# Kernel tuning notes

Measured on AMD Instinct MI355X. Metric: run time of the kernel, lower is better.

The kernel has to match this reference:

```python
import jax, jax.numpy as jnp
import numpy as np


def setup_inputs() -> dict:
    key = jax.random.key(0)
    k1, k2 = jax.random.split(key)
    B, P, C, N = 32, 3, 512, 1024
    input_data1 = jax.random.normal(k1, (B, P, C, N), dtype=jnp.float32)
    input_data2 = jax.random.normal(k2, (B, P, C, N), dtype=jnp.float32)
    return {"input_data1": input_data1, "input_data2": input_data2}


def reference(input_data1, input_data2):
    # HorizontalComparisonModel.compare_algorithm_method4 (the only path used):
    # permute [B,P,C,N] -> [B,P,N,C], reshape to [B, P*N, C] pairs of C-dim vectors.
    B = input_data1.shape[0]
    x = jnp.transpose(input_data1, (0, 1, 3, 2)).reshape(B, -1, input_data1.shape[2])
    y = jnp.transpose(input_data2, (0, 1, 3, 2)).reshape(B, -1, input_data2.shape[2])
    d = x - y                                   # [B, pairs, C]
    l1 = jnp.sum(jnp.abs(d), axis=-1)           # temp31: L1 distance
    sq_l2 = jnp.sum(d * d, axis=-1)             # temp21: squared L2 distance
    # Original stacks [temp31, temp21, temp31] (L1 appears twice; cosine unused).
    out = jnp.stack([l1, sq_l2, l1], axis=-1)   # [B, pairs, 3]
    return out.reshape(B, -1)
```

## Files before the change

kernel.cpp:

```cpp
#include <hip/hip_runtime.h>

constexpr int B = 32, P = 3, C = 512, N = 1024;
constexpr int G = B * P;
constexpr int CSPLIT = 16;
constexpr int CCHUNK = C / CSPLIT;
constexpr size_t WS_NEED = (size_t)CSPLIT * G * N * 2 * sizeof(float);

__global__ __launch_bounds__(256) void dist_partial(
    const float* __restrict__ x1, const float* __restrict__ x2,
    float* __restrict__ ws)
{
    const int g     = blockIdx.x / CSPLIT;
    const int chunk = blockIdx.x % CSPLIT;
    const int t     = threadIdx.x;

    const float4* pa = (const float4*)(x1 + (size_t)g * C * N)
                       + (size_t)chunk * CCHUNK * (N / 4) + t;
    const float4* pb = (const float4*)(x2 + (size_t)g * C * N)
                       + (size_t)chunk * CCHUNK * (N / 4) + t;

    float4 l1 = make_float4(0.f, 0.f, 0.f, 0.f);
    float4 l2 = make_float4(0.f, 0.f, 0.f, 0.f);

    #pragma unroll
    for (int j = 0; j < CCHUNK; j += 4) {
        const float4 a0 = pa[0 * (N / 4)];
        const float4 a1 = pa[1 * (N / 4)];
        const float4 a2 = pa[2 * (N / 4)];
        const float4 a3 = pa[3 * (N / 4)];
        const float4 b0 = pb[0 * (N / 4)];
        const float4 b1 = pb[1 * (N / 4)];
        const float4 b2 = pb[2 * (N / 4)];
        const float4 b3 = pb[3 * (N / 4)];
        pa += N;
        pb += N;
        float d;
        d = a0.x - b0.x; l1.x += fabsf(d); l2.x = fmaf(d, d, l2.x);
        d = a0.y - b0.y; l1.y += fabsf(d); l2.y = fmaf(d, d, l2.y);
        d = a0.z - b0.z; l1.z += fabsf(d); l2.z = fmaf(d, d, l2.z);
        d = a0.w - b0.w; l1.w += fabsf(d); l2.w = fmaf(d, d, l2.w);
        d = a1.x - b1.x; l1.x += fabsf(d); l2.x = fmaf(d, d, l2.x);
        d = a1.y - b1.y; l1.y += fabsf(d); l2.y = fmaf(d, d, l2.y);
        d = a1.z - b1.z; l1.z += fabsf(d); l2.z = fmaf(d, d, l2.z);
        d = a1.w - b1.w; l1.w += fabsf(d); l2.w = fmaf(d, d, l2.w);
        d = a2.x - b2.x; l1.x += fabsf(d); l2.x = fmaf(d, d, l2.x);
        d = a2.y - b2.y; l1.y += fabsf(d); l2.y = fmaf(d, d, l2.y);
        d = a2.z - b2.z; l1.z += fabsf(d); l2.z = fmaf(d, d, l2.z);
        d = a2.w - b2.w; l1.w += fabsf(d); l2.w = fmaf(d, d, l2.w);
        d = a3.x - b3.x; l1.x += fabsf(d); l2.x = fmaf(d, d, l2.x);
        d = a3.y - b3.y; l1.y += fabsf(d); l2.y = fmaf(d, d, l2.y);
        d = a3.z - b3.z; l1.z += fabsf(d); l2.z = fmaf(d, d, l2.z);
        d = a3.w - b3.w; l1.w += fabsf(d); l2.w = fmaf(d, d, l2.w);
    }

    float4* wout = (float4*)ws + ((size_t)(chunk * G + g) * N) / 2 + 2 * t;
    wout[0] = make_float4(l1.x, l2.x, l1.y, l2.y);
    wout[1] = make_float4(l1.z, l2.z, l1.w, l2.w);
}

__global__ __launch_bounds__(256) void dist_combine(
    const float* __restrict__ ws, float* __restrict__ out)
{
    const int idx = blockIdx.x * 256 + threadIdx.x;
    const float2* ws2 = (const float2*)ws;
    float l1 = 0.f, l2 = 0.f;
    #pragma unroll
    for (int chunk = 0; chunk < CSPLIT; ++chunk) {
        const float2 v = ws2[(size_t)chunk * G * N + idx];
        l1 += v.x;
        l2 += v.y;
    }
    out[3 * (size_t)idx + 0] = l1;
    out[3 * (size_t)idx + 1] = l2;
    out[3 * (size_t)idx + 2] = l1;
}

__global__ __launch_bounds__(256) void dist_atomic(
    const float* __restrict__ x1, const float* __restrict__ x2,
    float* __restrict__ out)
{
    const int g     = blockIdx.x / CSPLIT;
    const int chunk = blockIdx.x % CSPLIT;
    const int t     = threadIdx.x;
    const float4* a = (const float4*)(x1 + (size_t)g * C * N) + t;
    const float4* b = (const float4*)(x2 + (size_t)g * C * N) + t;
    const int c0 = chunk * CCHUNK;
    float4 l1 = make_float4(0.f, 0.f, 0.f, 0.f);
    float4 l2 = make_float4(0.f, 0.f, 0.f, 0.f);
    for (int c = c0; c < c0 + CCHUNK; ++c) {
        const float4 av = a[(size_t)c * (N / 4)];
        const float4 bv = b[(size_t)c * (N / 4)];
        float d;
        d = av.x - bv.x; l1.x += fabsf(d); l2.x = fmaf(d, d, l2.x);
        d = av.y - bv.y; l1.y += fabsf(d); l2.y = fmaf(d, d, l2.y);
        d = av.z - bv.z; l1.z += fabsf(d); l2.z = fmaf(d, d, l2.z);
        d = av.w - bv.w; l1.w += fabsf(d); l2.w = fmaf(d, d, l2.w);
    }
    const size_t obase = ((size_t)g * N + 4 * (size_t)t) * 3;
    const float l1v[4] = {l1.x, l1.y, l1.z, l1.w};
    const float l2v[4] = {l2.x, l2.y, l2.z, l2.w};
    #pragma unroll
    for (int i = 0; i < 4; ++i) {
        atomicAdd(&out[obase + 3 * i + 0], l1v[i]);
        atomicAdd(&out[obase + 3 * i + 1], l2v[i]);
        atomicAdd(&out[obase + 3 * i + 2], l1v[i]);
    }
}

extern "C" void kernel_launch(void* const* d_in, const int* in_sizes, int n_in,
                              void* d_out, int out_size, void* d_ws, size_t ws_size,
                              hipStream_t stream) {
    const float* x1 = (const float*)d_in[0];
    const float* x2 = (const float*)d_in[1];
    float* out = (float*)d_out;

    if (ws_size >= WS_NEED) {
        dist_partial<<<G * CSPLIT, 256, 0, stream>>>(x1, x2, (float*)d_ws);
        dist_combine<<<(G * N) / 256, 256, 0, stream>>>((const float*)d_ws, out);
    } else {
        hipMemsetAsync(d_out, 0, (size_t)out_size * sizeof(float), stream);
        dist_atomic<<<G * CSPLIT, 256, 0, stream>>>(x1, x2, out);
    }
}
```

Before: 392.9 us.

## Software-pipeline row loads and double channel split with templated CSPLIT

The partial-reduction kernel now prefetches the next group of rows into registers while it computes on the current group. Both kernels are templated on the channel split, and a split of 32 is preferred when the workspace is large enough, which doubles the block count. A launch-bounds occupancy hint is also added. The aim is more memory-level parallelism for this bandwidth-bound reduction, at the cost of a larger workspace and more combine traffic.

```diff
diff --git a/kernel.cpp b/kernel.cpp
--- a/kernel.cpp
+++ b/kernel.cpp
@@ -2,14 +2,21 @@
 
 constexpr int B = 32, P = 3, C = 512, N = 1024;
 constexpr int G = B * P;
-constexpr int CSPLIT = 16;
-constexpr int CCHUNK = C / CSPLIT;
-constexpr size_t WS_NEED = (size_t)CSPLIT * G * N * 2 * sizeof(float);
 
-__global__ __launch_bounds__(256) void dist_partial(
+constexpr size_t ws_need(int csplit) {
+    return (size_t)csplit * G * N * 2 * sizeof(float);
+}
+
+template <int CSPLIT>
+__global__ __launch_bounds__(256, 4) void dist_partial(
     const float* __restrict__ x1, const float* __restrict__ x2,
     float* __restrict__ ws)
 {
+    constexpr int CCHUNK = C / CSPLIT;
+    constexpr int R = 4;
+    constexpr int NJ = CCHUNK / R;
+    static_assert(CCHUNK % R == 0, "chunk must be multiple of stage rows");
+
     const int g     = blockIdx.x / CSPLIT;
     const int chunk = blockIdx.x % CSPLIT;
     const int t     = threadIdx.x;
@@ -22,35 +29,44 @@
     float4 l1 = make_float4(0.f, 0.f, 0.f, 0.f);
     float4 l2 = make_float4(0.f, 0.f, 0.f, 0.f);
 
+    float4 ca[R], cb[R], na[R], nb[R];
+
     #pragma unroll
-    for (int j = 0; j < CCHUNK; j += 4) {
-        const float4 a0 = pa[0 * (N / 4)];
-        const float4 a1 = pa[1 * (N / 4)];
-        const float4 a2 = pa[2 * (N / 4)];
-        const float4 a3 = pa[3 * (N / 4)];
-        const float4 b0 = pb[0 * (N / 4)];
-        const float4 b1 = pb[1 * (N / 4)];
-        const float4 b2 = pb[2 * (N / 4)];
-        const float4 b3 = pb[3 * (N / 4)];
-        pa += N;
-        pb += N;
-        float d;
-        d = a0.x - b0.x; l1.x += fabsf(d); l2.x = fmaf(d, d, l2.x);
-        d = a0.y - b0.y; l1.y += fabsf(d); l2.y = fmaf(d, d, l2.y);
-        d = a0.z - b0.z; l1.z += fabsf(d); l2.z = fmaf(d, d, l2.z);
-        d = a0.w - b0.w; l1.w += fabsf(d); l2.w = fmaf(d, d, l2.w);
-        d = a1.x - b1.x; l1.x += fabsf(d); l2.x = fmaf(d, d, l2.x);
-        d = a1.y - b1.y; l1.y += fabsf(d); l2.y = fmaf(d, d, l2.y);
-        d = a1.z - b1.z; l1.z += fabsf(d); l2.z = fmaf(d, d, l2.z);
-        d = a1.w - b1.w; l1.w += fabsf(d); l2.w = fmaf(d, d, l2.w);
-        d = a2.x - b2.x; l1.x += fabsf(d); l2.x = fmaf(d, d, l2.x);
-        d = a2.y - b2.y; l1.y += fabsf(d); l2.y = fmaf(d, d, l2.y);
-        d = a2.z - b2.z; l1.z += fabsf(d); l2.z = fmaf(d, d, l2.z);
-        d = a2.w - b2.w; l1.w += fabsf(d); l2.w = fmaf(d, d, l2.w);
-        d = a3.x - b3.x; l1.x += fabsf(d); l2.x = fmaf(d, d, l2.x);
-        d = a3.y - b3.y; l1.y += fabsf(d); l2.y = fmaf(d, d, l2.y);
-        d = a3.z - b3.z; l1.z += fabsf(d); l2.z = fmaf(d, d, l2.z);
-        d = a3.w - b3.w; l1.w += fabsf(d); l2.w = fmaf(d, d, l2.w);
+    for (int r = 0; r < R; ++r) {
+        ca[r] = pa[r * (N / 4)];
+        cb[r] = pb[r * (N / 4)];
+    }
+    pa += R * (N / 4);
+    pb += R * (N / 4);
+
+    #pragma unroll
+    for (int j = 0; j < NJ; ++j) {
+        if (j + 1 < NJ) {
+            #pragma unroll
+            for (int r = 0; r < R; ++r) {
+                na[r] = pa[r * (N / 4)];
+                nb[r] = pb[r * (N / 4)];
+            }
+            pa += R * (N / 4);
+            pb += R * (N / 4);
+        }
+
+        #pragma unroll
+        for (int r = 0; r < R; ++r) {
+            float d;
+            d = ca[r].x - cb[r].x; l1.x += fabsf(d); l2.x = fmaf(d, d, l2.x);
+            d = ca[r].y - cb[r].y; l1.y += fabsf(d); l2.y = fmaf(d, d, l2.y);
+            d = ca[r].z - cb[r].z; l1.z += fabsf(d); l2.z = fmaf(d, d, l2.z);
+            d = ca[r].w - cb[r].w; l1.w += fabsf(d); l2.w = fmaf(d, d, l2.w);
+        }
+
+        if (j + 1 < NJ) {
+            #pragma unroll
+            for (int r = 0; r < R; ++r) {
+                ca[r] = na[r];
+                cb[r] = nb[r];
+            }
+        }
     }
 
     float4* wout = (float4*)ws + ((size_t)(chunk * G + g) * N) / 2 + 2 * t;
@@ -58,6 +74,7 @@
     wout[1] = make_float4(l1.z, l2.z, l1.w, l2.w);
 }
 
+template <int CSPLIT>
 __global__ __launch_bounds__(256) void dist_combine(
     const float* __restrict__ ws, float* __restrict__ out)
 {
@@ -75,19 +92,21 @@
     out[3 * (size_t)idx + 2] = l1;
 }
 
+constexpr int FB_CSPLIT = 16;
+constexpr int FB_CCHUNK = C / FB_CSPLIT;
 __global__ __launch_bounds__(256) void dist_atomic(
     const float* __restrict__ x1, const float* __restrict__ x2,
     float* __restrict__ out)
 {
-    const int g     = blockIdx.x / CSPLIT;
-    const int chunk = blockIdx.x % CSPLIT;
+    const int g     = blockIdx.x / FB_CSPLIT;
+    const int chunk = blockIdx.x % FB_CSPLIT;
     const int t     = threadIdx.x;
     const float4* a = (const float4*)(x1 + (size_t)g * C * N) + t;
     const float4* b = (const float4*)(x2 + (size_t)g * C * N) + t;
-    const int c0 = chunk * CCHUNK;
+    const int c0 = chunk * FB_CCHUNK;
     float4 l1 = make_float4(0.f, 0.f, 0.f, 0.f);
     float4 l2 = make_float4(0.f, 0.f, 0.f, 0.f);
-    for (int c = c0; c < c0 + CCHUNK; ++c) {
+    for (int c = c0; c < c0 + FB_CCHUNK; ++c) {
         const float4 av = a[(size_t)c * (N / 4)];
         const float4 bv = b[(size_t)c * (N / 4)];
         float d;
@@ -114,11 +133,14 @@
     const float* x2 = (const float*)d_in[1];
     float* out = (float*)d_out;
 
-    if (ws_size >= WS_NEED) {
-        dist_partial<<<G * CSPLIT, 256, 0, stream>>>(x1, x2, (float*)d_ws);
-        dist_combine<<<(G * N) / 256, 256, 0, stream>>>((const float*)d_ws, out);
+    if (ws_size >= ws_need(32)) {
+        dist_partial<32><<<G * 32, 256, 0, stream>>>(x1, x2, (float*)d_ws);
+        dist_combine<32><<<(G * N) / 256, 256, 0, stream>>>((const float*)d_ws, out);
+    } else if (ws_size >= ws_need(16)) {
+        dist_partial<16><<<G * 16, 256, 0, stream>>>(x1, x2, (float*)d_ws);
+        dist_combine<16><<<(G * N) / 256, 256, 0, stream>>>((const float*)d_ws, out);
     } else {
         hipMemsetAsync(d_out, 0, (size_t)out_size * sizeof(float), stream);
-        dist_atomic<<<G * CSPLIT, 256, 0, stream>>>(x1, x2, out);
+        dist_atomic<<<G * FB_CSPLIT, 256, 0, stream>>>(x1, x2, out);
     }
 }
```

Result: no change. 394.3 us (+0.4%).
